# Kernel optimization log

Measured on AMD Instinct MI355X. Metric: run time of the kernel, lower is better.

Reference implementation:

```python
import jax, jax.numpy as jnp
import numpy as np

B, S, HID = 2, 2048, 2048
NH, NKV, D = 32, 4, 64
N_REP = NH // NKV
EPS = 1e-6
ROPE_THETA = 10000.0


def _rotate_half(x):
    h = x.shape[-1] // 2
    return jnp.concatenate([-x[..., h:], x[..., :h]], axis=-1)


def _rmsnorm(x, gamma):
    # RMSNorm over last dim (head_dim)
    return x * jax.lax.rsqrt(jnp.mean(x * x, axis=-1, keepdims=True) + EPS) * gamma


def setup_inputs() -> dict:
    key = jax.random.key(0)
    ks = jax.random.split(key, 8)
    hidden_states = jax.random.normal(ks[0], (B, S, HID), dtype=jnp.float32)
    # rotary cos/sin tables, shape [B, S, D]
    pos = jnp.arange(S, dtype=jnp.float32)
    inv_freq = 1.0 / (ROPE_THETA ** (jnp.arange(0, D, 2, dtype=jnp.float32) / D))
    freqs = pos[:, None] * inv_freq[None, :]            # [S, D/2]
    emb = jnp.concatenate([freqs, freqs], axis=-1)      # [S, D]
    cos = jnp.broadcast_to(jnp.cos(emb)[None], (B, S, D))
    sin = jnp.broadcast_to(jnp.sin(emb)[None], (B, S, D))
    sc = 0.02
    Wq = jax.random.normal(ks[1], (NH * D, HID), dtype=jnp.float32) * sc
    Wk = jax.random.normal(ks[2], (NKV * D, HID), dtype=jnp.float32) * sc
    Wv = jax.random.normal(ks[3], (NKV * D, HID), dtype=jnp.float32) * sc
    Wg = jax.random.normal(ks[4], (NH * D, HID), dtype=jnp.float32) * sc
    Wo = jax.random.normal(ks[5], (HID, NH * D), dtype=jnp.float32) * sc
    q_gamma = jnp.ones((D,), dtype=jnp.float32)
    k_gamma = jnp.ones((D,), dtype=jnp.float32)
    return dict(hidden_states=hidden_states, cos=cos, sin=sin,
                Wq=Wq, Wk=Wk, Wv=Wv, Wg=Wg, Wo=Wo,
                q_gamma=q_gamma, k_gamma=k_gamma)


def reference(hidden_states, cos, sin, Wq, Wk, Wv, Wg, Wo, q_gamma, k_gamma):
    b, s, _ = hidden_states.shape
    q = (hidden_states @ Wq.T).reshape(b, s, NH, D)
    k = (hidden_states @ Wk.T).reshape(b, s, NKV, D)
    v = (hidden_states @ Wv.T).reshape(b, s, NKV, D)
    gate = hidden_states @ Wg.T                       # [B, S, NH*D]
    # per-head RMSNorm on q/k
    q = _rmsnorm(q, q_gamma)
    k = _rmsnorm(k, k_gamma)
    # [B, H, S, D]
    q = q.transpose(0, 2, 1, 3)
    k = k.transpose(0, 2, 1, 3)
    v = v.transpose(0, 2, 1, 3)
    # RoPE (unsqueeze_dim=1)
    c = cos[:, None, :, :]
    sn = sin[:, None, :, :]
    q = q * c + _rotate_half(q) * sn
    k = k * c + _rotate_half(k) * sn
    # GQA: repeat kv heads
    kr = jnp.repeat(k, N_REP, axis=1)
    vr = jnp.repeat(v, N_REP, axis=1)
    scaling = D ** -0.5
    scores = jnp.einsum('bhqd,bhkd->bhqk', q, kr) * scaling
    w = jax.nn.softmax(scores.astype(jnp.float32), axis=-1).astype(q.dtype)
    out = jnp.einsum('bhqk,bhkd->bhqd', w, vr)
    out = out.transpose(0, 2, 1, 3).reshape(b, s, NH * D)
    out = out * jax.nn.sigmoid(gate)
    return out @ Wo.T
```

## Files before the change

kernel.cpp:

```cpp
#include <hip/hip_runtime.h>


#define LOG2E 1.44269504088896340736f

typedef __attribute__((ext_vector_type(4))) float f32x4;
typedef __attribute__((ext_vector_type(8))) short bf16x8;

__device__ __forceinline__ float bf2f(unsigned short u) {
  union { unsigned u; float f; } x; x.u = ((unsigned)u) << 16; return x.f;
}
__device__ __forceinline__ unsigned short f2bf(float f) {
  union { float f; unsigned u; } x; x.f = f;
  unsigned r = x.u + 0x7fffu + ((x.u >> 16) & 1u);
  return (unsigned short)(r >> 16);
}

__device__ __forceinline__ void async16(void* lds, const void* g) {
  __builtin_amdgcn_global_load_lds(
      (const __attribute__((address_space(1))) unsigned*)g,
      (__attribute__((address_space(3))) unsigned*)lds, 16, 0, 0);
}
__device__ __forceinline__ void lds_fence() {
  __asm__ volatile("s_waitcnt lgkmcnt(0)" ::: "memory");
}

__global__ __launch_bounds__(256) void cvt_all(
    const float* __restrict__ s0, const float* __restrict__ s1,
    const float* __restrict__ s2, const float* __restrict__ s3,
    const float* __restrict__ s4, const float* __restrict__ s5,
    unsigned short* __restrict__ d0, unsigned short* __restrict__ d1,
    unsigned short* __restrict__ d2, unsigned short* __restrict__ d3,
    unsigned short* __restrict__ d4, unsigned short* __restrict__ d5) {
  const long total = 5505024;
  const long stride = (long)gridDim.x * 256;
  for (long i = (long)blockIdx.x * 256 + threadIdx.x; i < total; i += stride) {
    const float* s; unsigned short* d; long off;
    if      (i < 2097152) { s = s0; d = d0; off = 0; }
    else if (i < 3145728) { s = s1; d = d1; off = 2097152; }
    else if (i < 3276800) { s = s2; d = d2; off = 3145728; }
    else if (i < 3407872) { s = s3; d = d3; off = 3276800; }
    else if (i < 4456448) { s = s4; d = d4; off = 3407872; }
    else                  { s = s5; d = d5; off = 4456448; }
    long j = i - off;
    float4 v = reinterpret_cast<const float4*>(s)[j];
    ushort4 u;
    u.x = f2bf(v.x); u.y = f2bf(v.y); u.z = f2bf(v.z); u.w = f2bf(v.w);
    reinterpret_cast<ushort4*>(d)[j] = u;
  }
}

__device__ __forceinline__ void gemm_main_big(
    const unsigned short* __restrict__ A, const unsigned short* __restrict__ W,
    int m0, int n0, unsigned short* lds, f32x4 acc[4][4]) {
  const int tid = threadIdx.x;
  const int w = tid >> 6, l = tid & 63, quad = l >> 4, l16 = l & 15;
  const int l7 = l16 & 7;
  const int wm = (w & 1) * 64, wn = (w >> 1) * 64;
  const int rlo = tid >> 3, ch = tid & 7;

  const f32x4 Z4 = {0.f, 0.f, 0.f, 0.f};
#pragma unroll
  for (int i = 0; i < 4; i++)
#pragma unroll
    for (int j = 0; j < 4; j++) acc[i][j] = Z4;

  const unsigned short* gA = A + (size_t)(m0 + rlo) * 2048 + ((ch ^ (rlo & 7)) * 8);
  const unsigned short* gB = W + (size_t)(n0 + rlo) * 2048 + ((ch ^ (rlo & 7)) * 8);

  int arow[4], brow[4];
#pragma unroll
  for (int mt = 0; mt < 4; mt++) arow[mt] = (wm + mt * 16 + l16) * 64;
#pragma unroll
  for (int nt = 0; nt < 4; nt++) brow[nt] = (wn + nt * 16 + l16) * 64;
  const int x0 = (quad ^ l7) * 8;
  const int x1 = ((4 + quad) ^ l7) * 8;

  unsigned short* const bA = lds;
  unsigned short* const bB = lds + 16384;

  async16(bA + tid * 8,          gA);
  async16(bA + 4096 + tid * 8,   gA + 131072);
  async16(bB + tid * 8,          gB);
  async16(bB + 4096 + tid * 8,   gB + 131072);
  async16(bB + 8192 + tid * 8,   gB + 262144);
  async16(bB + 12288 + tid * 8,  gB + 393216);
  async16(bB + 16384 + tid * 8,  gB + 64);
  async16(bB + 20480 + tid * 8,  gB + 131072 + 64);
  async16(bB + 24576 + tid * 8,  gB + 262144 + 64);
  async16(bB + 28672 + tid * 8,  gB + 393216 + 64);
  __asm__ volatile("s_waitcnt vmcnt(4)" ::: "memory");
  __builtin_amdgcn_s_barrier();

  int cb = 0;
  for (int t = 0; t < 32; ++t) {
    unsigned short* cbA = bA + (t & 1) * 8192;
    unsigned short* cbB = bB + cb * 16384;

    if (t < 31) {
      unsigned short* nA = bA + ((t + 1) & 1) * 8192;
      const int ko = (t + 1) * 64;
      async16(nA + tid * 8,        gA + ko);
      async16(nA + 4096 + tid * 8, gA + 131072 + ko);
    }
    bf16x8 a0[4], b0[4];
#pragma unroll
    for (int mt = 0; mt < 4; mt++)
      a0[mt] = *(const bf16x8*)&cbA[arow[mt] + x0];
#pragma unroll
    for (int nt = 0; nt < 4; nt++)
      b0[nt] = *(const bf16x8*)&cbB[brow[nt] + x0];
    __builtin_amdgcn_s_barrier();
    __asm__ volatile("s_waitcnt lgkmcnt(0)" ::: "memory");
    __builtin_amdgcn_sched_barrier(0);
    __builtin_amdgcn_s_setprio(1);
#pragma unroll
    for (int mt = 0; mt < 4; mt++)
#pragma unroll
      for (int nt = 0; nt < 4; nt++)
        acc[mt][nt] = __builtin_amdgcn_mfma_f32_16x16x32_bf16(
            a0[mt], b0[nt], acc[mt][nt], 0, 0, 0);
    __builtin_amdgcn_s_setprio(0);
    __builtin_amdgcn_s_barrier();

    if (t < 30) {
      int nb = cb + 2; if (nb >= 3) nb -= 3;
      unsigned short* nB = bB + nb * 16384;
      const int ko = (t + 2) * 64;
      async16(nB + tid * 8,         gB + ko);
      async16(nB + 4096 + tid * 8,  gB + 131072 + ko);
      async16(nB + 8192 + tid * 8,  gB + 262144 + ko);
      async16(nB + 12288 + tid * 8, gB + 393216 + ko);
    }
    bf16x8 a1[4], b1[4];
#pragma unroll
    for (int mt = 0; mt < 4; mt++)
      a1[mt] = *(const bf16x8*)&cbA[arow[mt] + x1];
#pragma unroll
    for (int nt = 0; nt < 4; nt++)
      b1[nt] = *(const bf16x8*)&cbB[brow[nt] + x1];
    __builtin_amdgcn_s_barrier();
    __asm__ volatile("s_waitcnt lgkmcnt(0)" ::: "memory");
    __builtin_amdgcn_sched_barrier(0);
    __builtin_amdgcn_s_setprio(1);
#pragma unroll
    for (int mt = 0; mt < 4; mt++)
#pragma unroll
      for (int nt = 0; nt < 4; nt++)
        acc[mt][nt] = __builtin_amdgcn_mfma_f32_16x16x32_bf16(
            a1[mt], b1[nt], acc[mt][nt], 0, 0, 0);
    __builtin_amdgcn_s_setprio(0);
    if (t < 30) {
      __asm__ volatile("s_waitcnt vmcnt(4)" ::: "memory");
    } else if (t == 30) {
      __asm__ volatile("s_waitcnt vmcnt(0)" ::: "memory");
    }
    __builtin_amdgcn_s_barrier();
    cb++; if (cb == 3) cb = 0;
  }
}

__global__ __launch_bounds__(512, 2) void gemm_qkvg(
    const unsigned short* __restrict__ X,
    const unsigned short* __restrict__ Wq, const unsigned short* __restrict__ Wk,
    const unsigned short* __restrict__ Wv, const unsigned short* __restrict__ Wg,
    const float* __restrict__ cosb, const float* __restrict__ sinb,
    const float* __restrict__ qg, const float* __restrict__ kg,
    unsigned short* __restrict__ Qn, unsigned short* __restrict__ Kn,
    unsigned short* __restrict__ Vt, unsigned short* __restrict__ gate) {
  __shared__ __attribute__((aligned(16))) unsigned short lds[65536];
  const int ny = blockIdx.y;
  const unsigned short* W; int n0, type;
  if (ny < 8)       { W = Wq; n0 = ny * 256;        type = 0; }
  else if (ny == 8) { W = Wk; n0 = 0;               type = 1; }
  else if (ny == 9) { W = Wv; n0 = 0;               type = 2; }
  else              { W = Wg; n0 = (ny - 10) * 256; type = 3; }
  const int m0 = blockIdx.x * 128;

  f32x4 acc[4][4];
  gemm_main_big(X, W, m0, n0, lds, acc);

  const int tid = threadIdx.x;
  const int w = tid >> 6, l = tid & 63, quad = l >> 4, l16 = l & 15;
  const int wm = (w & 1) * 64, wn = (w >> 1) * 64;

  if (type == 3) {
#pragma unroll
    for (int mt = 0; mt < 4; mt++)
#pragma unroll
      for (int r = 0; r < 4; r++) {
        int row = m0 + wm + mt * 16 + quad * 4 + r;
#pragma unroll
        for (int nt = 0; nt < 4; nt++)
          gate[(size_t)row * 2048 + n0 + wn + nt * 16 + l16] =
              f2bf(acc[mt][nt][r]);
      }
    return;
  }
  if (type == 2) {
#pragma unroll
    for (int mt = 0; mt < 4; mt++)
#pragma unroll
      for (int r = 0; r < 4; r++) {
        int row = m0 + wm + mt * 16 + quad * 4 + r;
        int b = row >> 11, s = row & 2047;
#pragma unroll
        for (int nt = 0; nt < 4; nt++) {
          int col = wn + nt * 16 + l16;
          int kvh = col >> 6, d = col & 63;
          Vt[((size_t)(b * 4 + kvh) * 64 + d) * 2048 + s] =
              f2bf(acc[mt][nt][r]);
        }
      }
    return;
  }

  const float* gamma = (type == 0) ? qg : kg;
  const float scale  = (type == 0) ? 0.125f : LOG2E;
  const int hb = (n0 + wn) >> 6;
  float gv[4];
#pragma unroll
  for (int nt = 0; nt < 4; nt++) gv[nt] = gamma[nt * 16 + l16];

#pragma unroll
  for (int mt = 0; mt < 4; mt++)
#pragma unroll
    for (int r = 0; r < 4; r++) {
      int row = m0 + wm + mt * 16 + quad * 4 + r;
      float ss = 0.f;
#pragma unroll
      for (int nt = 0; nt < 4; nt++) {
        float v = acc[mt][nt][r]; ss += v * v;
      }
#pragma unroll
      for (int off = 1; off < 16; off <<= 1) ss += __shfl_xor(ss, off);
      float rr = rsqrtf(ss * (1.0f / 64.0f) + 1e-6f);
      float xn[4];
#pragma unroll
      for (int nt = 0; nt < 4; nt++) xn[nt] = acc[mt][nt][r] * rr * gv[nt];
      int b = row >> 11, s = row & 2047;
      unsigned short* dst = (type == 0)
          ? Qn + ((size_t)(b * 32 + hb) * 2048 + s) * 64
          : Kn + ((size_t)(b * 4 + hb) * 2048 + s) * 64;
#pragma unroll
      for (int nt = 0; nt < 4; nt++) {
        int d = nt * 16 + l16;
        float rot = (nt < 2) ? -xn[nt ^ 2] : xn[nt ^ 2];
        float cv = cosb[(size_t)row * 64 + d];
        float sv = sinb[(size_t)row * 64 + d];
        dst[d] = f2bf((xn[nt] * cv + rot * sv) * scale);
      }
    }
}

__global__ __launch_bounds__(512, 2) void gemm_out_k(
    const unsigned short* __restrict__ A, const unsigned short* __restrict__ W,
    float* __restrict__ C) {
  __shared__ __attribute__((aligned(16))) unsigned short lds[65536];
  const int m0 = blockIdx.x * 128, n0 = blockIdx.y * 256;
  f32x4 acc[4][4];
  gemm_main_big(A, W, m0, n0, lds, acc);
  const int tid = threadIdx.x;
  const int w = tid >> 6, l = tid & 63, quad = l >> 4, l16 = l & 15;
  const int wm = (w & 1) * 64, wn = (w >> 1) * 64;
#pragma unroll
  for (int mt = 0; mt < 4; mt++)
#pragma unroll
    for (int nt = 0; nt < 4; nt++) {
      int row = m0 + wm + mt * 16 + quad * 4;
      int col = n0 + wn + nt * 16 + l16;
#pragma unroll
      for (int r = 0; r < 4; r++)
        C[(size_t)(row + r) * 2048 + col] = acc[mt][nt][r];
    }
}

__global__ __launch_bounds__(256, 4) void attn(
    const unsigned short* __restrict__ Qn, const unsigned short* __restrict__ Kn,
    const unsigned short* __restrict__ Vt, const unsigned short* __restrict__ gate,
    unsigned short* __restrict__ act) {
  __shared__ __attribute__((aligned(16))) unsigned short smem[20480];
  unsigned short* Ps = smem + 16384;

  const int tid = threadIdx.x, w = tid >> 6, l = tid & 63;
  const int quad = l >> 4, l16 = l & 15, l7 = l16 & 7;
  const int bh = blockIdx.y, b = bh >> 5, h = bh & 31, kvh = h >> 3;
  const int q0 = blockIdx.x * 128;

  const unsigned short* Qg = Qn + ((size_t)(b * 32 + h) * 2048 + q0) * 64;
  const unsigned short* Kg = Kn + (size_t)(b * 4 + kvh) * 2048 * 64;
  const unsigned short* Vg = Vt + (size_t)(b * 4 + kvh) * 64 * 2048;
  unsigned short* Pw = Ps + w * 1024;

  const int kq_src = ((tid & 7) ^ ((tid >> 3) & 7)) * 8;

#pragma unroll
  for (int i = 0; i < 4; i++)
    async16(smem + i * 2048 + tid * 8,
            Qg + (size_t)(i * 32 + (tid >> 3)) * 64 + kq_src);
  __syncthreads();
  bf16x8 qf[2][2];
#pragma unroll
  for (int mt = 0; mt < 2; mt++)
#pragma unroll
    for (int ks = 0; ks < 2; ks++) {
      int row = w * 32 + mt * 16 + l16;
      qf[mt][ks] = *(const bf16x8*)&smem[row * 64 + ((ks * 4 + quad) ^ l7) * 8];
    }
  __syncthreads();

  const f32x4 Z4 = {0.f, 0.f, 0.f, 0.f};
  f32x4 O[2][4];
  float lp[2][4];
#pragma unroll
  for (int mt = 0; mt < 2; mt++) {
#pragma unroll
    for (int nt = 0; nt < 4; nt++) O[mt][nt] = Z4;
#pragma unroll
    for (int r = 0; r < 4; r++) lp[mt][r] = 0.f;
  }

#pragma unroll
  for (int i = 0; i < 2; i++) {
    async16(smem + i * 2048 + tid * 8,
            Kg + (size_t)(i * 32 + (tid >> 3)) * 64 + kq_src);
    async16(smem + 4096 + i * 2048 + tid * 8,
            Vg + (size_t)(i * 32 + (tid >> 3)) * 2048 + kq_src);
  }

  for (int kt = 0; kt < 32; kt++) {
    __syncthreads();

    if (kt < 31) {
      unsigned short* nb = smem + ((kt + 1) & 1) * 8192;
      const int s1 = (kt + 1) * 64;
#pragma unroll
      for (int i = 0; i < 2; i++) {
        async16(nb + i * 2048 + tid * 8,
                Kg + (size_t)(s1 + i * 32 + (tid >> 3)) * 64 + kq_src);
        async16(nb + 4096 + i * 2048 + tid * 8,
                Vg + (size_t)(i * 32 + (tid >> 3)) * 2048 + s1 + kq_src);
      }
    }

    unsigned short* Ks  = smem + (kt & 1) * 8192;
    unsigned short* Vts = Ks + 4096;

    f32x4 sc[2][4];
#pragma unroll
    for (int mt = 0; mt < 2; mt++)
#pragma unroll
      for (int nt = 0; nt < 4; nt++) sc[mt][nt] = Z4;
    __builtin_amdgcn_s_setprio(1);
#pragma unroll
    for (int nt = 0; nt < 4; nt++) {
      int row = nt * 16 + l16;
      bf16x8 kf0 = *(const bf16x8*)&Ks[row * 64 + (quad ^ l7) * 8];
      bf16x8 kf1 = *(const bf16x8*)&Ks[row * 64 + ((4 + quad) ^ l7) * 8];
#pragma unroll
      for (int mt = 0; mt < 2; mt++) {
        sc[mt][nt] = __builtin_amdgcn_mfma_f32_16x16x32_bf16(qf[mt][0], kf0, sc[mt][nt], 0, 0, 0);
        sc[mt][nt] = __builtin_amdgcn_mfma_f32_16x16x32_bf16(qf[mt][1], kf1, sc[mt][nt], 0, 0, 0);
      }
    }
    __builtin_amdgcn_s_setprio(0);

#pragma unroll
    for (int ks2 = 0; ks2 < 2; ks2++) {
#pragma unroll
      for (int mt = 0; mt < 2; mt++)
#pragma unroll
        for (int ntl = 0; ntl < 2; ntl++) {
          int nt = ks2 * 2 + ntl;
#pragma unroll
          for (int r = 0; r < 4; r++) {
            float p = __builtin_amdgcn_exp2f(sc[mt][nt][r]);
            union { float f; unsigned u; } x; x.f = p;
            union { unsigned u; float f; } t; t.u = x.u & 0xffff0000u;
            lp[mt][r] += t.f;
            int q = mt * 16 + quad * 4 + r;
            int c = ntl * 2 + (l16 >> 3);
            int phys = c ^ ((q >> 1) & 3);
            Pw[q * 32 + phys * 8 + l7] = (unsigned short)(x.u >> 16);
          }
        }
      lds_fence();

      bf16x8 pf[2];
#pragma unroll
      for (int mt = 0; mt < 2; mt++) {
        int q = mt * 16 + l16;
        int phys = quad ^ ((l16 >> 1) & 3);
        pf[mt] = *(const bf16x8*)&Pw[q * 32 + phys * 8];
      }
      __builtin_amdgcn_s_setprio(1);
#pragma unroll
      for (int nt2 = 0; nt2 < 4; nt2++) {
        int d = nt2 * 16 + l16;
        bf16x8 vf = *(const bf16x8*)&Vts[d * 64 + ((ks2 * 4 + quad) ^ l7) * 8];
#pragma unroll
        for (int mt = 0; mt < 2; mt++)
          O[mt][nt2] = __builtin_amdgcn_mfma_f32_16x16x32_bf16(
              pf[mt], vf, O[mt][nt2], 0, 0, 0);
      }
      __builtin_amdgcn_s_setprio(0);
      lds_fence();
    }
  }

#pragma unroll
  for (int mt = 0; mt < 2; mt++)
#pragma unroll
    for (int r = 0; r < 4; r++) {
      float s = lp[mt][r];
#pragma unroll
      for (int off = 1; off < 16; off <<= 1) s += __shfl_xor(s, off);
      lp[mt][r] = s;
    }

#pragma unroll
  for (int mt = 0; mt < 2; mt++) {
    float inv[4];
#pragma unroll
    for (int r = 0; r < 4; r++) inv[r] = 1.0f / lp[mt][r];
#pragma unroll
    for (int nt = 0; nt < 4; nt++)
#pragma unroll
      for (int r = 0; r < 4; r++) {
        int srow = q0 + w * 32 + mt * 16 + quad * 4 + r;
        int col = h * 64 + nt * 16 + l16;
        size_t off = (size_t)(b * 2048 + srow) * 2048 + col;
        float g = bf2f(gate[off]);
        float sig = 1.0f / (1.0f + __builtin_amdgcn_exp2f(-g * LOG2E));
        act[off] = f2bf(O[mt][nt][r] * inv[r] * sig);
      }
  }
}

extern "C" void kernel_launch(void* const* d_in, const int* in_sizes, int n_in,
                              void* d_out, int out_size, void* d_ws, size_t ws_size,
                              hipStream_t stream) {
  const float* hid  = (const float*)d_in[0];
  const float* cosb = (const float*)d_in[1];
  const float* sinb = (const float*)d_in[2];
  const float* Wq   = (const float*)d_in[3];
  const float* Wk   = (const float*)d_in[4];
  const float* Wv   = (const float*)d_in[5];
  const float* Wg   = (const float*)d_in[6];
  const float* Wo   = (const float*)d_in[7];
  const float* qg   = (const float*)d_in[8];
  const float* kg   = (const float*)d_in[9];
  float* out = (float*)d_out;

  char* ws = (char*)d_ws;
  unsigned short* Xb   = (unsigned short*)(ws);
  unsigned short* WqB  = (unsigned short*)(ws + 16777216);
  unsigned short* WkB  = (unsigned short*)(ws + 25165824);
  unsigned short* WvB  = (unsigned short*)(ws + 26214400);
  unsigned short* WgB  = (unsigned short*)(ws + 27262976);
  unsigned short* WoB  = (unsigned short*)(ws + 35651584);
  unsigned short* gate = (unsigned short*)(ws + 44040192);
  unsigned short* Qn   = (unsigned short*)(ws + 60817408);
  unsigned short* Kn   = (unsigned short*)(ws + 77594624);
  unsigned short* Vt   = (unsigned short*)(ws + 79691776);
  unsigned short* act = WqB;

  cvt_all<<<dim3(2048), dim3(256), 0, stream>>>(
      hid, Wq, Wk, Wv, Wg, Wo, Xb, WqB, WkB, WvB, WgB, WoB);

  gemm_qkvg<<<dim3(32, 18), dim3(512), 0, stream>>>(
      Xb, WqB, WkB, WvB, WgB, cosb, sinb, qg, kg, Qn, Kn, Vt, gate);

  attn<<<dim3(16, 64), dim3(256), 0, stream>>>(Qn, Kn, Vt, gate, act);

  gemm_out_k<<<dim3(32, 8), dim3(512), 0, stream>>>(act, WoB, out);
}
```

Measured before the change: 372.4 us.

## Halve GEMM K-tile to 32 with triple-buffered A/B and smaller LDS footprint

Restructures the QKVG projection GEMM main loop to use a K step of 32 instead of 64. A and B are now both triple-buffered in a unified ring with a single prefetch and barrier per iteration, and the LDS swizzle changes to suit 4 chunks per row. LDS per block drops from 128KB to 72KB and launch bounds rise to 4 blocks per CU, aiming for higher occupancy and better latency hiding. The trade-off is twice as many iterations and barriers per K pass, and the occupancy hint may push register pressure toward spills.

```diff
diff --git a/kernel.cpp b/kernel.cpp
--- a/kernel.cpp
+++ b/kernel.cpp
@@ -54,9 +54,8 @@
     int m0, int n0, unsigned short* lds, f32x4 acc[4][4]) {
   const int tid = threadIdx.x;
   const int w = tid >> 6, l = tid & 63, quad = l >> 4, l16 = l & 15;
-  const int l7 = l16 & 7;
   const int wm = (w & 1) * 64, wn = (w >> 1) * 64;
-  const int rlo = tid >> 3, ch = tid & 7;
+  const int rlo = tid >> 2, ch = tid & 3;
 
   const f32x4 Z4 = {0.f, 0.f, 0.f, 0.f};
 #pragma unroll
@@ -64,51 +63,50 @@
 #pragma unroll
     for (int j = 0; j < 4; j++) acc[i][j] = Z4;
 
-  const unsigned short* gA = A + (size_t)(m0 + rlo) * 2048 + ((ch ^ (rlo & 7)) * 8);
-  const unsigned short* gB = W + (size_t)(n0 + rlo) * 2048 + ((ch ^ (rlo & 7)) * 8);
+  const unsigned short* gA =
+      A + (size_t)(m0 + rlo) * 2048 + ((ch ^ ((rlo >> 1) & 3)) * 8);
+  const unsigned short* gB =
+      W + (size_t)(n0 + rlo) * 2048 + ((ch ^ ((rlo >> 1) & 3)) * 8);
 
   int arow[4], brow[4];
 #pragma unroll
-  for (int mt = 0; mt < 4; mt++) arow[mt] = (wm + mt * 16 + l16) * 64;
-#pragma unroll
-  for (int nt = 0; nt < 4; nt++) brow[nt] = (wn + nt * 16 + l16) * 64;
-  const int x0 = (quad ^ l7) * 8;
-  const int x1 = ((4 + quad) ^ l7) * 8;
+  for (int mt = 0; mt < 4; mt++) arow[mt] = (wm + mt * 16 + l16) * 32;
+#pragma unroll
+  for (int nt = 0; nt < 4; nt++) brow[nt] = (wn + nt * 16 + l16) * 32;
+  const int fx = (quad ^ ((l16 >> 1) & 3)) * 8;
 
   unsigned short* const bA = lds;
-  unsigned short* const bB = lds + 16384;
-
-  async16(bA + tid * 8,          gA);
-  async16(bA + 4096 + tid * 8,   gA + 131072);
-  async16(bB + tid * 8,          gB);
-  async16(bB + 4096 + tid * 8,   gB + 131072);
-  async16(bB + 8192 + tid * 8,   gB + 262144);
-  async16(bB + 12288 + tid * 8,  gB + 393216);
-  async16(bB + 16384 + tid * 8,  gB + 64);
-  async16(bB + 20480 + tid * 8,  gB + 131072 + 64);
-  async16(bB + 24576 + tid * 8,  gB + 262144 + 64);
-  async16(bB + 28672 + tid * 8,  gB + 393216 + 64);
-  __asm__ volatile("s_waitcnt vmcnt(4)" ::: "memory");
+  unsigned short* const bB = lds + 12288;
+
+#pragma unroll
+  for (int tt = 0; tt < 2; ++tt) {
+    const int ko = tt * 32;
+    async16(bA + tt * 4096 + tid * 8,        gA + ko);
+    async16(bB + tt * 8192 + tid * 8,        gB + ko);
+    async16(bB + tt * 8192 + 4096 + tid * 8, gB + 262144 + ko);
+  }
+  __asm__ volatile("s_waitcnt vmcnt(3)" ::: "memory");
   __builtin_amdgcn_s_barrier();
 
   int cb = 0;
-  for (int t = 0; t < 32; ++t) {
-    unsigned short* cbA = bA + (t & 1) * 8192;
-    unsigned short* cbB = bB + cb * 16384;
-
-    if (t < 31) {
-      unsigned short* nA = bA + ((t + 1) & 1) * 8192;
-      const int ko = (t + 1) * 64;
-      async16(nA + tid * 8,        gA + ko);
-      async16(nA + 4096 + tid * 8, gA + 131072 + ko);
-    }
-    bf16x8 a0[4], b0[4];
+  for (int t = 0; t < 64; ++t) {
+    unsigned short* cA = bA + cb * 4096;
+    unsigned short* cB = bB + cb * 8192;
+
+    if (t < 62) {
+      int nb = cb + 2; if (nb >= 3) nb -= 3;
+      const int ko = (t + 2) * 32;
+      async16(bA + nb * 4096 + tid * 8,        gA + ko);
+      async16(bB + nb * 8192 + tid * 8,        gB + ko);
+      async16(bB + nb * 8192 + 4096 + tid * 8, gB + 262144 + ko);
+    }
+    bf16x8 af[4], bf[4];
 #pragma unroll
     for (int mt = 0; mt < 4; mt++)
-      a0[mt] = *(const bf16x8*)&cbA[arow[mt] + x0];
+      af[mt] = *(const bf16x8*)&cA[arow[mt] + fx];
 #pragma unroll
     for (int nt = 0; nt < 4; nt++)
-      b0[nt] = *(const bf16x8*)&cbB[brow[nt] + x0];
+      bf[nt] = *(const bf16x8*)&cB[brow[nt] + fx];
     __builtin_amdgcn_s_barrier();
     __asm__ volatile("s_waitcnt lgkmcnt(0)" ::: "memory");
     __builtin_amdgcn_sched_barrier(0);
@@ -118,40 +116,11 @@
 #pragma unroll
       for (int nt = 0; nt < 4; nt++)
         acc[mt][nt] = __builtin_amdgcn_mfma_f32_16x16x32_bf16(
-            a0[mt], b0[nt], acc[mt][nt], 0, 0, 0);
+            af[mt], bf[nt], acc[mt][nt], 0, 0, 0);
     __builtin_amdgcn_s_setprio(0);
-    __builtin_amdgcn_s_barrier();
-
-    if (t < 30) {
-      int nb = cb + 2; if (nb >= 3) nb -= 3;
-      unsigned short* nB = bB + nb * 16384;
-      const int ko = (t + 2) * 64;
-      async16(nB + tid * 8,         gB + ko);
-      async16(nB + 4096 + tid * 8,  gB + 131072 + ko);
-      async16(nB + 8192 + tid * 8,  gB + 262144 + ko);
-      async16(nB + 12288 + tid * 8, gB + 393216 + ko);
-    }
-    bf16x8 a1[4], b1[4];
-#pragma unroll
-    for (int mt = 0; mt < 4; mt++)
-      a1[mt] = *(const bf16x8*)&cbA[arow[mt] + x1];
-#pragma unroll
-    for (int nt = 0; nt < 4; nt++)
-      b1[nt] = *(const bf16x8*)&cbB[brow[nt] + x1];
-    __builtin_amdgcn_s_barrier();
-    __asm__ volatile("s_waitcnt lgkmcnt(0)" ::: "memory");
-    __builtin_amdgcn_sched_barrier(0);
-    __builtin_amdgcn_s_setprio(1);
-#pragma unroll
-    for (int mt = 0; mt < 4; mt++)
-#pragma unroll
-      for (int nt = 0; nt < 4; nt++)
-        acc[mt][nt] = __builtin_amdgcn_mfma_f32_16x16x32_bf16(
-            a1[mt], b1[nt], acc[mt][nt], 0, 0, 0);
-    __builtin_amdgcn_s_setprio(0);
-    if (t < 30) {
-      __asm__ volatile("s_waitcnt vmcnt(4)" ::: "memory");
-    } else if (t == 30) {
+    if (t < 62) {
+      __asm__ volatile("s_waitcnt vmcnt(3)" ::: "memory");
+    } else if (t == 62) {
       __asm__ volatile("s_waitcnt vmcnt(0)" ::: "memory");
     }
     __builtin_amdgcn_s_barrier();
@@ -159,7 +128,7 @@
   }
 }
 
-__global__ __launch_bounds__(512, 2) void gemm_qkvg(
+__global__ __launch_bounds__(512, 4) void gemm_qkvg(
     const unsigned short* __restrict__ X,
     const unsigned short* __restrict__ Wq, const unsigned short* __restrict__ Wk,
     const unsigned short* __restrict__ Wv, const unsigned short* __restrict__ Wg,
@@ -167,7 +136,7 @@
     const float* __restrict__ qg, const float* __restrict__ kg,
     unsigned short* __restrict__ Qn, unsigned short* __restrict__ Kn,
     unsigned short* __restrict__ Vt, unsigned short* __restrict__ gate) {
-  __shared__ __attribute__((aligned(16))) unsigned short lds[65536];
+  __shared__ __attribute__((aligned(16))) unsigned short lds[36864];
   const int ny = blockIdx.y;
   const unsigned short* W; int n0, type;
   if (ny < 8)       { W = Wq; n0 = ny * 256;        type = 0; }
```

Measured after the change: 382.7 us. 1.03x slower.
